# Optimization experiments

Hardware: AMD Instinct MI355X
Metric: run time of the kernel (lower is better)

The kernel has to match this reference:

```python
import jax, jax.numpy as jnp
import numpy as np

EPS = 1e-5
NEG_INF = -1e30


def layer_norm_seq(x, gamma, beta):
    # Faithful to the custom LayerNorm: normalizes over dim=1 (the T axis of
    # [B, T, C]) with UNBIASED variance (torch.var default), then scales by
    # gamma/beta of shape [C] broadcast over the last axis.
    m = jnp.mean(x, axis=1, keepdims=True)
    v = jnp.var(x, axis=1, keepdims=True, ddof=1)
    return gamma * (x - m) / jnp.sqrt(v + EPS) + beta


def setup_inputs() -> dict:
    key = jax.random.key(0)
    B, T, C, H = 4, 1024, 1024, 16
    hd = C // H  # 64
    ks = jax.random.split(key, 10)
    s_in = 1.0 / np.sqrt(C)
    s_ff = 1.0 / np.sqrt(4 * C)
    return {
        "x": jax.random.normal(ks[0], (B, T, C), dtype=jnp.float32),
        # NOTE: Head uses self.key(x) for BOTH q and k; the query Linear is
        # dead code, so only key/value weights are materialized.
        "Wk": jax.random.uniform(ks[1], (H, C, hd), minval=-s_in, maxval=s_in, dtype=jnp.float32),
        "Wv": jax.random.uniform(ks[2], (H, C, hd), minval=-s_in, maxval=s_in, dtype=jnp.float32),
        "Wp": jax.random.uniform(ks[3], (C, C), minval=-s_in, maxval=s_in, dtype=jnp.float32),
        "bp": jnp.zeros((C,), dtype=jnp.float32),
        "W1": jax.random.uniform(ks[4], (4 * C, C), minval=-s_in, maxval=s_in, dtype=jnp.float32),
        "b1": jnp.zeros((4 * C,), dtype=jnp.float32),
        "W2": jax.random.uniform(ks[5], (C, 4 * C), minval=-s_ff, maxval=s_ff, dtype=jnp.float32),
        "b2": jnp.zeros((C,), dtype=jnp.float32),
        "g1": jnp.ones((C,), dtype=jnp.float32),
        "beta1": jnp.zeros((C,), dtype=jnp.float32),
        "g2": jnp.ones((C,), dtype=jnp.float32),
        "beta2": jnp.zeros((C,), dtype=jnp.float32),
    }


def reference(x, Wk, Wv, Wp, bp, W1, b1, W2, b2, g1, beta1, g2, beta2):
    B, T, C = x.shape
    H, _, hd = Wk.shape
    scale = hd ** -0.5

    # --- self-attention sublayer (pre-LN over sequence axis) ---
    h = layer_norm_seq(x, g1, beta1)
    # q and k BOTH use the key projection (faithful to the original bug).
    qk = jnp.einsum("btc,hcd->bhtd", h, Wk)          # [B,H,T,hd]
    v = jnp.einsum("btc,hcd->bhtd", h, Wv)           # [B,H,T,hd]
    wei = jnp.einsum("bhtd,bhsd->bhts", qk, qk) * scale  # [B,H,T,T]
    causal = jnp.tril(jnp.ones((T, T), dtype=bool))
    wei = jnp.where(causal, wei, NEG_INF)
    wei = jax.nn.softmax(wei, axis=-1)
    attn = jnp.einsum("bhts,bhsd->bthd", wei, v).reshape(B, T, C)
    attn = attn @ Wp.T + bp
    x = x + attn

    # --- feed-forward sublayer ---
    h2 = layer_norm_seq(x, g2, beta2)
    ff = jax.nn.relu(h2 @ W1.T + b1) @ W2.T + b2
    return x + ff
```

## Files before the change

### kernel.cpp

```cpp
#include <hip/hip_runtime.h>
#include <stdint.h>


#define BDIM 256

typedef __attribute__((ext_vector_type(8))) __bf16 bf16x8;
typedef __attribute__((ext_vector_type(4))) float f32x4;

__device__ __forceinline__ unsigned short f2bf(float f) {
    unsigned u = __float_as_uint(f);
    u += 0x7fff + ((u >> 16) & 1);
    return (unsigned short)(u >> 16);
}

__device__ __forceinline__ void gload_lds16(const void* g, void* l) {
    __builtin_amdgcn_global_load_lds(
        (const __attribute__((address_space(1))) void*)g,
        (__attribute__((address_space(3))) void*)l, 16, 0, 0);
}

__global__ void k_cast_bf16(const float* __restrict__ in, unsigned short* __restrict__ out, int n4) {
    int i = blockIdx.x * BDIM + threadIdx.x;
    if (i >= n4) return;
    float4 v = ((const float4*)in)[i];
    ushort4 o;
    o.x = f2bf(v.x); o.y = f2bf(v.y); o.z = f2bf(v.z); o.w = f2bf(v.w);
    ((ushort4*)out)[i] = o;
}

__global__ void k_headT(const float* __restrict__ W, unsigned short* __restrict__ out) {
    __shared__ float tile[64][65];
    const int tid = threadIdx.x;
    const int c0 = blockIdx.x * 64, h = blockIdx.y;
    const float* src = W + ((long)h << 16) + (long)c0 * 64;
    #pragma unroll
    for (int j = 0; j < 16; ++j) {
        int idx = j * 256 + tid;
        tile[idx >> 6][idx & 63] = src[idx];
    }
    __syncthreads();
    #pragma unroll
    for (int j = 0; j < 16; ++j) {
        int idx = j * 256 + tid;
        int d = idx >> 6, c = idx & 63;
        out[(long)(h * 64 + d) * 1024 + c0 + c] = f2bf(tile[c][d]);
    }
}

__global__ void k_ln_part(const float* __restrict__ x, float* __restrict__ psum, float* __restrict__ psq) {
    int c = blockIdx.x * BDIM + threadIdx.x;
    int tc = blockIdx.y, b = blockIdx.z;
    const float* p = x + ((long)b << 20) + ((long)tc * 128) * 1024 + c;
    float s = 0.f, ss = 0.f;
    for (int t = 0; t < 128; ++t) {
        float v = p[t * 1024];
        s += v; ss += v * v;
    }
    int o = (b * 8 + tc) * 1024 + c;
    psum[o] = s; psq[o] = ss;
}

__global__ void k_ln_fin(const float* __restrict__ psum, const float* __restrict__ psq,
                         float* __restrict__ mean, float* __restrict__ rstd) {
    int i = blockIdx.x * BDIM + threadIdx.x;
    int b = i >> 10, c = i & 1023;
    float s = 0.f, ss = 0.f;
    for (int j = 0; j < 8; ++j) {
        s  += psum[(b * 8 + j) * 1024 + c];
        ss += psq[(b * 8 + j) * 1024 + c];
    }
    float m = s * (1.0f / 1024.0f);
    float var = (ss - 1024.0f * m * m) * (1.0f / 1023.0f);
    mean[i] = m;
    rstd[i] = rsqrtf(var + 1e-5f);
}

__global__ void k_ln_apply(const float* __restrict__ x, const float* __restrict__ mean,
                           const float* __restrict__ rstd, const float* __restrict__ g,
                           const float* __restrict__ beta, unsigned short* __restrict__ out) {
    int i = blockIdx.x * BDIM + threadIdx.x;
    int flat = i << 2;
    int b = flat >> 20, c = flat & 1023;
    float4 xv = ((const float4*)x)[i];
    float4 mv = *(const float4*)&mean[(b << 10) + c];
    float4 rv = *(const float4*)&rstd[(b << 10) + c];
    float4 gv = *(const float4*)&g[c];
    float4 bv = *(const float4*)&beta[c];
    ushort4 o;
    o.x = f2bf(gv.x * (xv.x - mv.x) * rv.x + bv.x);
    o.y = f2bf(gv.y * (xv.y - mv.y) * rv.y + bv.y);
    o.z = f2bf(gv.z * (xv.z - mv.z) * rv.z + bv.z);
    o.w = f2bf(gv.w * (xv.w - mv.w) * rv.w + bv.w);
    ((ushort4*)out)[i] = o;
}

__global__ void k_addbias(const float* __restrict__ res, const float* __restrict__ bias,
                          float* __restrict__ out) {
    int i = blockIdx.x * BDIM + threadIdx.x;
    int c = (i << 2) & 1023;
    float4 r = ((const float4*)res)[i];
    float4 bv = *(const float4*)&bias[c];
    r.x += bv.x; r.y += bv.y; r.z += bv.z; r.w += bv.w;
    ((float4*)out)[i] = r;
}

template <int EPI>
__global__ __launch_bounds__(256, 3) void k_gemm_bt(
    const unsigned short* __restrict__ A, const unsigned short* __restrict__ B,
    void* __restrict__ Cv, const float* __restrict__ bias, const float* __restrict__ res,
    int N, int K, int ldA, int ldB, long sA, long sB, long sC)
{
    __shared__ __align__(16) unsigned short As[2][128 * 32];
    __shared__ __align__(16) unsigned short Bs[2][128 * 32];
    const int tid = threadIdx.x;
    const int wave = tid >> 6, lane = tid & 63;
    const long bz = blockIdx.z;
    const int m0 = blockIdx.y * 128, n0 = blockIdx.x * 128;

    const int srow = wave * 16 + (lane >> 2);
    const int kbs = (lane & 3) ^ ((srow >> 1) & 3);
    const unsigned short* gA0 = A + bz * sA + (long)(m0 + srow) * ldA + kbs * 8;
    const unsigned short* gB0 = B + bz * sB + (long)(n0 + srow) * ldB + kbs * 8;
    const long rowoffA = (long)64 * ldA;
    const long rowoffB = (long)64 * ldB;
    const int lofs = wave * 512;

    f32x4 acc[4][4] = {};
    const int wm = (wave >> 1) * 64, wn = (wave & 1) * 64;
    const int lr = lane & 15, lg = lane >> 4;
    const int aoff = (lg ^ ((lr >> 1) & 3)) * 8;

    auto stage = [&](int kt, int buf) {
        gload_lds16(gA0 + kt, &As[buf][lofs]);
        gload_lds16(gA0 + rowoffA + kt, &As[buf][2048 + lofs]);
        gload_lds16(gB0 + kt, &Bs[buf][lofs]);
        gload_lds16(gB0 + rowoffB + kt, &Bs[buf][2048 + lofs]);
    };

    stage(0, 0);
    asm volatile("s_waitcnt vmcnt(0)" ::: "memory");
    __builtin_amdgcn_s_barrier();
    __builtin_amdgcn_sched_barrier(0);

    int cur = 0;
    for (int kt = 0; kt < K; kt += 32) {
        const int nxt = cur ^ 1;
        if (kt + 32 < K) stage(kt + 32, nxt);
        bf16x8 af[4], bfr[4];
        #pragma unroll
        for (int i = 0; i < 4; ++i) {
            af[i]  = *(const bf16x8*)&As[cur][(wm + i * 16 + lr) * 32 + aoff];
            bfr[i] = *(const bf16x8*)&Bs[cur][(wn + i * 16 + lr) * 32 + aoff];
        }
        #pragma unroll
        for (int i = 0; i < 4; ++i)
            #pragma unroll
            for (int j = 0; j < 4; ++j)
                acc[i][j] = __builtin_amdgcn_mfma_f32_16x16x32_bf16(af[i], bfr[j], acc[i][j], 0, 0, 0);
        asm volatile("s_waitcnt vmcnt(0)" ::: "memory");
        __builtin_amdgcn_s_barrier();
        __builtin_amdgcn_sched_barrier(0);
        cur = nxt;
    }

    const int cr0 = lg * 4;
    #pragma unroll
    for (int mi = 0; mi < 4; ++mi) {
        #pragma unroll
        for (int r = 0; r < 4; ++r) {
            const int row = m0 + wm + mi * 16 + cr0 + r;
            const long rb = bz * sC + (long)row * N;
            #pragma unroll
            for (int nj = 0; nj < 4; ++nj) {
                const int col = n0 + wn + nj * 16 + lr;
                float v = acc[mi][nj][r];
                if (EPI == 0) {
                    ((unsigned short*)Cv)[rb + col] = f2bf(v);
                } else if (EPI == 1) {
                    ((float*)Cv)[rb + col] = v + bias[col] + res[rb + col];
                } else {
                    v += bias[col];
                    ((unsigned short*)Cv)[rb + col] = f2bf(v > 0.f ? v : 0.f);
                }
            }
        }
    }
}

template <int EPI>
__global__ __launch_bounds__(512, 2) void k_gemm256(
    const unsigned short* __restrict__ A, const unsigned short* __restrict__ B,
    void* __restrict__ Cv, const float* __restrict__ bias,
    int N, int K, int ldA, int ldB)
{
    __shared__ __align__(16) unsigned short As[2][2][128 * 64];
    __shared__ __align__(16) unsigned short Bs[2][2][128 * 64];
    const int tid = threadIdx.x;
    const int wv = tid >> 6, l = tid & 63;
    const int m0 = blockIdx.y * 256, n0 = blockIdx.x * 256;
    const long koff = (long)blockIdx.z * K;

    const int lr = l & 15, lg = l >> 4;

    const int srow = wv * 16 + (l >> 3);
    const int g0 = (l & 7) ^ (l >> 4);
    const int g1 = (l & 7) ^ (4 + (l >> 4));
    const unsigned short* pA = A + koff + (long)(m0 + srow) * ldA;
    const unsigned short* pB = B + koff + (long)(n0 + srow) * ldB;
    const long l8A = (long)8 * ldA, l128A = (long)128 * ldA;
    const long l8B = (long)8 * ldB, l128B = (long)128 * ldB;
    const int dst0 = wv * 1024;

    auto stage = [&](int k0, int d) {
        #pragma unroll
        for (int h = 0; h < 2; ++h) {
            gload_lds16(pA + (long)h * l128A + k0 + g0 * 8, &As[d][h][dst0]);
            gload_lds16(pA + (long)h * l128A + l8A + k0 + g1 * 8, &As[d][h][dst0 + 512]);
            gload_lds16(pB + (long)h * l128B + k0 + g0 * 8, &Bs[d][h][dst0]);
            gload_lds16(pB + (long)h * l128B + l8B + k0 + g1 * 8, &Bs[d][h][dst0 + 512]);
        }
    };

    f32x4 acc[8][4] = {};
    const int wh = wv >> 2;
    const int bh = (wv & 3) >> 1;
    const int brow0 = (wv & 1) * 64;
    const int swz = (lr >> 1) & 7;

    stage(0, 0);

    const int nt = K >> 6;
    int cur = 0;
    for (int t = 0; t < nt; ++t) {
        asm volatile("s_waitcnt vmcnt(0)" ::: "memory");
        __builtin_amdgcn_s_barrier();
        __builtin_amdgcn_sched_barrier(0);
        if (t + 1 < nt) stage((t + 1) << 6, cur ^ 1);
        const unsigned short* Ah = &As[cur][wh][0];
        const unsigned short* Bh = &Bs[cur][bh][0];
        #pragma unroll
        for (int ks = 0; ks < 2; ++ks) {
            const int kb = ((ks * 4 + lg) ^ swz) * 8;
            bf16x8 af[8], bfr[4];
            #pragma unroll
            for (int fm = 0; fm < 8; ++fm)
                af[fm] = *(const bf16x8*)&Ah[(fm * 16 + lr) * 64 + kb];
            #pragma unroll
            for (int fn = 0; fn < 4; ++fn)
                bfr[fn] = *(const bf16x8*)&Bh[(brow0 + fn * 16 + lr) * 64 + kb];
            asm volatile("s_waitcnt lgkmcnt(0)" ::: "memory");
            __builtin_amdgcn_sched_barrier(0);
            __builtin_amdgcn_s_setprio(1);
            #pragma unroll
            for (int fm = 0; fm < 8; ++fm)
                #pragma unroll
                for (int fn = 0; fn < 4; ++fn)
                    acc[fm][fn] = __builtin_amdgcn_mfma_f32_16x16x32_bf16(af[fm], bfr[fn], acc[fm][fn], 0, 0, 0);
            __builtin_amdgcn_s_setprio(0);
            __builtin_amdgcn_sched_barrier(0);
        }
        cur ^= 1;
    }

    const int wm = (wv >> 2) * 128, wn = (wv & 3) * 64;
    #pragma unroll
    for (int fm = 0; fm < 8; ++fm) {
        #pragma unroll
        for (int r = 0; r < 4; ++r) {
            const int row = m0 + wm + fm * 16 + lg * 4 + r;
            const long rb = (long)row * N;
            #pragma unroll
            for (int fn = 0; fn < 4; ++fn) {
                const int col = n0 + wn + fn * 16 + lr;
                float v = acc[fm][fn][r];
                if (EPI == 2) {
                    v += bias[col];
                    ((unsigned short*)Cv)[rb + col] = f2bf(v > 0.f ? v : 0.f);
                } else {
                    atomicAdd(&((float*)Cv)[rb + col], v);
                }
            }
        }
    }
}

#define CEXP 0.18033688f
#define PSTRIDE 72

__global__ __launch_bounds__(256, 2) void k_attn(
    const unsigned short* __restrict__ qk, const unsigned short* __restrict__ vt,
    unsigned short* __restrict__ ctx)
{
    __shared__ __align__(16) unsigned short Ks[64 * 64];
    __shared__ __align__(16) unsigned short Vs[64 * 64];
    __shared__ __align__(16) unsigned short P[4][16 * PSTRIDE];
    const int tid = threadIdx.x;
    const int wave = tid >> 6, lane = tid & 63;
    const int bh = blockIdx.x >> 3, pairIdx = blockIdx.x & 7;
    const int b = bh >> 4, h = bh & 15;
    const int lr = lane & 15, lg = lane >> 4;

    const int swz = (lr & 7) << 4;
    const int cby0 = (lg * 16) ^ swz;
    const int cby1 = (64 + lg * 16) ^ swz;
    const int srow_l = lane >> 3;
    const int scol = ((lane & 7) * 8) ^ (srow_l << 3);

    unsigned short* Pw = P[wave];
    char* KsB = (char*)Ks;
    char* VsB = (char*)Vs;
    const unsigned short* qbase = qk + ((long)b << 20) + h * 64;
    const unsigned short* vb    = vt + ((long)(b * 16 + h) << 16);

    #pragma unroll 1
    for (int phase = 0; phase < 2; ++phase) {
        const int qb = phase ? (15 - pairIdx) : pairIdx;
        const int q0 = qb << 6;
        const int qw = q0 + wave * 16;

        const unsigned short* qrow = qbase + (long)(qw + lr) * 1024 + lg * 8;
        const bf16x8 aq0 = *(const bf16x8*)qrow;
        const bf16x8 aq1 = *(const bf16x8*)(qrow + 32);

        f32x4 acc[4] = {};
        float mrow[4] = {-1e30f, -1e30f, -1e30f, -1e30f};
        float lrow[4] = {0.f, 0.f, 0.f, 0.f};

        for (int c = 0; c <= qb; ++c) {
            const int k0 = c << 6;
            __syncthreads();
            #pragma unroll
            for (int i = 0; i < 2; ++i) {
                const int row = i * 32 + wave * 8 + srow_l;
                gload_lds16(qbase + (long)(k0 + row) * 1024 + scol,
                            KsB + i * 4096 + wave * 1024);
                gload_lds16(vb + (long)row * 1024 + k0 + scol,
                            VsB + i * 4096 + wave * 1024);
            }
            __syncthreads();

            f32x4 s[4];
            #pragma unroll
            for (int t = 0; t < 4; ++t) {
                const int r = t * 16 + lr;
                bf16x8 bk0 = *(const bf16x8*)(KsB + r * 128 + cby0);
                bf16x8 bk1 = *(const bf16x8*)(KsB + r * 128 + cby1);
                f32x4 z = {};
                z = __builtin_amdgcn_mfma_f32_16x16x32_bf16(aq0, bk0, z, 0, 0, 0);
                s[t] = __builtin_amdgcn_mfma_f32_16x16x32_bf16(aq1, bk1, z, 0, 0, 0);
            }
            if (c == qb) {
                #pragma unroll
                for (int t = 0; t < 4; ++t) {
                    const int col = t * 16 + lr;
                    #pragma unroll
                    for (int r = 0; r < 4; ++r)
                        if (col > wave * 16 + lg * 4 + r) s[t][r] = -1e30f;
                }
            }
            float fac[4];
            #pragma unroll
            for (int r = 0; r < 4; ++r) {
                float v = fmaxf(fmaxf(s[0][r], s[1][r]), fmaxf(s[2][r], s[3][r]));
                v = fmaxf(v, __shfl_xor(v, 1));
                v = fmaxf(v, __shfl_xor(v, 2));
                v = fmaxf(v, __shfl_xor(v, 4));
                v = fmaxf(v, __shfl_xor(v, 8));
                float mn = fmaxf(mrow[r], v);
                fac[r] = exp2f((mrow[r] - mn) * CEXP);
                mrow[r] = mn;
            }
            float psum[4] = {0.f, 0.f, 0.f, 0.f};
            #pragma unroll
            for (int t = 0; t < 4; ++t) {
                #pragma unroll
                for (int r = 0; r < 4; ++r) {
                    float p = exp2f((s[t][r] - mrow[r]) * CEXP);
                    psum[r] += p;
                    Pw[(lg * 4 + r) * PSTRIDE + t * 16 + lr] = f2bf(p);
                }
            }
            #pragma unroll
            for (int r = 0; r < 4; ++r) {
                float v = psum[r];
                v += __shfl_xor(v, 1); v += __shfl_xor(v, 2);
                v += __shfl_xor(v, 4); v += __shfl_xor(v, 8);
                lrow[r] = lrow[r] * fac[r] + v;
            }
            #pragma unroll
            for (int ni = 0; ni < 4; ++ni)
                #pragma unroll
                for (int r = 0; r < 4; ++r)
                    acc[ni][r] *= fac[r];
            const bf16x8 pa0 = *(const bf16x8*)&Pw[lr * PSTRIDE + lg * 8];
            const bf16x8 pa1 = *(const bf16x8*)&Pw[lr * PSTRIDE + 32 + lg * 8];
            #pragma unroll
            for (int ni = 0; ni < 4; ++ni) {
                const int vr = ni * 16 + lr;
                bf16x8 bv0 = *(const bf16x8*)(VsB + vr * 128 + cby0);
                bf16x8 bv1 = *(const bf16x8*)(VsB + vr * 128 + cby1);
                acc[ni] = __builtin_amdgcn_mfma_f32_16x16x32_bf16(pa0, bv0, acc[ni], 0, 0, 0);
                acc[ni] = __builtin_amdgcn_mfma_f32_16x16x32_bf16(pa1, bv1, acc[ni], 0, 0, 0);
            }
        }

        unsigned short* crow = ctx + ((long)(b * 1024 + qw)) * 1024 + h * 64;
        #pragma unroll
        for (int r = 0; r < 4; ++r) {
            const float inv = 1.0f / lrow[r];
            #pragma unroll
            for (int ni = 0; ni < 4; ++ni)
                crow[(long)(lg * 4 + r) * 1024 + ni * 16 + lr] = f2bf(acc[ni][r] * inv);
        }
    }
}

extern "C" void kernel_launch(void* const* d_in, const int* in_sizes, int n_in,
                              void* d_out, int out_size, void* d_ws, size_t ws_size,
                              hipStream_t stream)
{
    const float* x   = (const float*)d_in[0];
    const float* Wk  = (const float*)d_in[1];
    const float* Wv  = (const float*)d_in[2];
    const float* Wp  = (const float*)d_in[3];
    const float* bp  = (const float*)d_in[4];
    const float* W1  = (const float*)d_in[5];
    const float* b1  = (const float*)d_in[6];
    const float* W2  = (const float*)d_in[7];
    const float* b2  = (const float*)d_in[8];
    const float* g1  = (const float*)d_in[9];
    const float* be1 = (const float*)d_in[10];
    const float* g2  = (const float*)d_in[11];
    const float* be2 = (const float*)d_in[12];
    float* out = (float*)d_out;

    char* ws = (char*)d_ws;
    const long MB = 1024 * 1024;
    unsigned short* BkT = (unsigned short*)(ws);
    unsigned short* WvT = (unsigned short*)(ws + 2 * MB);
    unsigned short* WpB = (unsigned short*)(ws + 4 * MB);
    unsigned short* W1B = (unsigned short*)(ws + 6 * MB);
    unsigned short* W2B = (unsigned short*)(ws + 14 * MB);
    unsigned short* hB  = (unsigned short*)(ws + 22 * MB);
    unsigned short* qkB = (unsigned short*)(ws + 30 * MB);
    unsigned short* VtB = (unsigned short*)(ws + 38 * MB);
    unsigned short* ctx = (unsigned short*)(ws + 46 * MB);
    unsigned short* ff1 = (unsigned short*)(ws + 30 * MB);
    float* x2   = (float*)(ws + 62 * MB);
    float* psum = (float*)(ws + 78 * MB);
    float* psq  = (float*)(ws + 78 * MB + 128 * 1024);
    float* mean = (float*)(ws + 78 * MB + 256 * 1024);
    float* rstd = (float*)(ws + 78 * MB + 272 * 1024);

    k_cast_bf16<<<1024, BDIM, 0, stream>>>(Wp, WpB, 262144);
    k_cast_bf16<<<4096, BDIM, 0, stream>>>(W1, W1B, 1048576);
    k_cast_bf16<<<4096, BDIM, 0, stream>>>(W2, W2B, 1048576);
    k_headT<<<dim3(16, 16), BDIM, 0, stream>>>(Wk, BkT);
    k_headT<<<dim3(16, 16), BDIM, 0, stream>>>(Wv, WvT);

    k_ln_part<<<dim3(4, 8, 4), BDIM, 0, stream>>>(x, psum, psq);
    k_ln_fin<<<16, BDIM, 0, stream>>>(psum, psq, mean, rstd);
    k_ln_apply<<<4096, BDIM, 0, stream>>>(x, mean, rstd, g1, be1, hB);

    k_gemm_bt<0><<<dim3(8, 32, 1), BDIM, 0, stream>>>(hB, BkT, qkB, nullptr, nullptr, 1024, 1024, 1024, 1024, 0, 0, 0);
    k_gemm_bt<0><<<dim3(8, 8, 4), BDIM, 0, stream>>>(WvT, hB, VtB, nullptr, nullptr, 1024, 1024, 1024, 1024, 0, MB, MB);

    k_attn<<<512, BDIM, 0, stream>>>(qkB, VtB, ctx);

    k_gemm_bt<1><<<dim3(8, 32, 1), BDIM, 0, stream>>>(ctx, WpB, x2, bp, x, 1024, 1024, 1024, 1024, 0, 0, 0);

    k_ln_part<<<dim3(4, 8, 4), BDIM, 0, stream>>>(x2, psum, psq);
    k_ln_fin<<<16, BDIM, 0, stream>>>(psum, psq, mean, rstd);
    k_ln_apply<<<4096, BDIM, 0, stream>>>(x2, mean, rstd, g2, be2, hB);

    k_gemm256<2><<<dim3(16, 16, 1), 512, 0, stream>>>(hB, W1B, ff1, b1, 4096, 1024, 1024, 1024);

    k_addbias<<<4096, BDIM, 0, stream>>>(x2, b2, out);
    k_gemm256<3><<<dim3(4, 16, 4), 512, 0, stream>>>(ff1, W2B, out, nullptr, 1024, 1024, 4096, 4096);
}
```

Before: 403.0 us.

## Deepen GEMM prefetch, split MFMA into quadrants, and remap workgroups across XCDs

The 256x256 GEMM now prefetches two k-tiles ahead and waits on a partial vmcnt instead of draining all loads, so global-to-LDS copies overlap more compute. Fragment loads and MFMA work are split into four quadrant phases separated by barriers, in a ping-pong style meant to interleave LDS reads with matrix ops. Workgroup IDs are remapped with a stride of 8 so neighbouring tiles land on the same XCD for L2 reuse. The extra barriers add sync overhead, and the remap assumes the grid size divides by 8.

Result: no change. 399.3 us (-0.9%).

```diff
diff --git a/kernel.cpp b/kernel.cpp
--- a/kernel.cpp
+++ b/kernel.cpp
@@ -197,7 +197,12 @@
     __shared__ __align__(16) unsigned short Bs[2][2][128 * 64];
     const int tid = threadIdx.x;
     const int wv = tid >> 6, l = tid & 63;
-    const int m0 = blockIdx.y * 256, n0 = blockIdx.x * 256;
+
+    const int gx = gridDim.x;
+    const int nwg = gx * gridDim.y;
+    int lin = blockIdx.y * gx + blockIdx.x;
+    lin = (lin & 7) * (nwg >> 3) + (lin >> 3);
+    const int m0 = (lin / gx) * 256, n0 = (lin % gx) * 256;
     const long koff = (long)blockIdx.z * K;
 
     const int lr = l & 15, lg = l >> 4;
@@ -223,43 +228,95 @@
 
     f32x4 acc[8][4] = {};
     const int wh = wv >> 2;
-    const int bh = (wv & 3) >> 1;
+    const int bhf = (wv & 3) >> 1;
     const int brow0 = (wv & 1) * 64;
     const int swz = (lr >> 1) & 7;
 
+    const int nt = K >> 6;
     stage(0, 0);
-
-    const int nt = K >> 6;
-    int cur = 0;
+    stage(64, 1);
+
     for (int t = 0; t < nt; ++t) {
-        asm volatile("s_waitcnt vmcnt(0)" ::: "memory");
+        const int d = t & 1;
+        if (t + 1 < nt) { asm volatile("s_waitcnt vmcnt(8)" ::: "memory"); }
+        else            { asm volatile("s_waitcnt vmcnt(0)" ::: "memory"); }
         __builtin_amdgcn_s_barrier();
         __builtin_amdgcn_sched_barrier(0);
-        if (t + 1 < nt) stage((t + 1) << 6, cur ^ 1);
-        const unsigned short* Ah = &As[cur][wh][0];
-        const unsigned short* Bh = &Bs[cur][bh][0];
-        #pragma unroll
-        for (int ks = 0; ks < 2; ++ks) {
-            const int kb = ((ks * 4 + lg) ^ swz) * 8;
-            bf16x8 af[8], bfr[4];
-            #pragma unroll
-            for (int fm = 0; fm < 8; ++fm)
-                af[fm] = *(const bf16x8*)&Ah[(fm * 16 + lr) * 64 + kb];
-            #pragma unroll
-            for (int fn = 0; fn < 4; ++fn)
-                bfr[fn] = *(const bf16x8*)&Bh[(brow0 + fn * 16 + lr) * 64 + kb];
-            asm volatile("s_waitcnt lgkmcnt(0)" ::: "memory");
-            __builtin_amdgcn_sched_barrier(0);
-            __builtin_amdgcn_s_setprio(1);
-            #pragma unroll
-            for (int fm = 0; fm < 8; ++fm)
-                #pragma unroll
-                for (int fn = 0; fn < 4; ++fn)
-                    acc[fm][fn] = __builtin_amdgcn_mfma_f32_16x16x32_bf16(af[fm], bfr[fn], acc[fm][fn], 0, 0, 0);
-            __builtin_amdgcn_s_setprio(0);
-            __builtin_amdgcn_sched_barrier(0);
-        }
-        cur ^= 1;
+        const unsigned short* Ah = &As[d][wh][0];
+        const unsigned short* Bh = &Bs[d][bhf][0];
+
+        bf16x8 aLo[4][2], aHi[4][2], b01[2][2], b23[2][2];
+        #pragma unroll
+        for (int fm = 0; fm < 4; ++fm)
+            #pragma unroll
+            for (int ks = 0; ks < 2; ++ks)
+                aLo[fm][ks] = *(const bf16x8*)&Ah[(fm * 16 + lr) * 64 + (((ks * 4 + lg) ^ swz) * 8)];
+        #pragma unroll
+        for (int fn = 0; fn < 2; ++fn)
+            #pragma unroll
+            for (int ks = 0; ks < 2; ++ks)
+                b01[fn][ks] = *(const bf16x8*)&Bh[(brow0 + fn * 16 + lr) * 64 + (((ks * 4 + lg) ^ swz) * 8)];
+        asm volatile("s_waitcnt lgkmcnt(0)" ::: "memory");
+        __builtin_amdgcn_sched_barrier(0);
+        __builtin_amdgcn_s_setprio(1);
+        #pragma unroll
+        for (int fm = 0; fm < 4; ++fm)
+            #pragma unroll
+            for (int fn = 0; fn < 2; ++fn)
+                #pragma unroll
+                for (int ks = 0; ks < 2; ++ks)
+                    acc[fm][fn] = __builtin_amdgcn_mfma_f32_16x16x32_bf16(aLo[fm][ks], b01[fn][ks], acc[fm][fn], 0, 0, 0);
+        __builtin_amdgcn_s_setprio(0);
+        __builtin_amdgcn_sched_barrier(0);
+        __builtin_amdgcn_s_barrier();
+        #pragma unroll
+        for (int fn = 0; fn < 2; ++fn)
+            #pragma unroll
+            for (int ks = 0; ks < 2; ++ks)
+                b23[fn][ks] = *(const bf16x8*)&Bh[(brow0 + (fn + 2) * 16 + lr) * 64 + (((ks * 4 + lg) ^ swz) * 8)];
+        asm volatile("s_waitcnt lgkmcnt(0)" ::: "memory");
+        __builtin_amdgcn_sched_barrier(0);
+        __builtin_amdgcn_s_setprio(1);
+        #pragma unroll
+        for (int fm = 0; fm < 4; ++fm)
+            #pragma unroll
+            for (int fn = 0; fn < 2; ++fn)
+                #pragma unroll
+                for (int ks = 0; ks < 2; ++ks)
+                    acc[fm][fn + 2] = __builtin_amdgcn_mfma_f32_16x16x32_bf16(aLo[fm][ks], b23[fn][ks], acc[fm][fn + 2], 0, 0, 0);
+        __builtin_amdgcn_s_setprio(0);
+        __builtin_amdgcn_sched_barrier(0);
+        __builtin_amdgcn_s_barrier();
+        #pragma unroll
+        for (int fm = 0; fm < 4; ++fm)
+            #pragma unroll
+            for (int ks = 0; ks < 2; ++ks)
+                aHi[fm][ks] = *(const bf16x8*)&Ah[((fm + 4) * 16 + lr) * 64 + (((ks * 4 + lg) ^ swz) * 8)];
+        asm volatile("s_waitcnt lgkmcnt(0)" ::: "memory");
+        __builtin_amdgcn_sched_barrier(0);
+        __builtin_amdgcn_s_setprio(1);
+        #pragma unroll
+        for (int fm = 0; fm < 4; ++fm)
+            #pragma unroll
+            for (int fn = 0; fn < 2; ++fn)
+                #pragma unroll
+                for (int ks = 0; ks < 2; ++ks)
+                    acc[fm + 4][fn + 2] = __builtin_amdgcn_mfma_f32_16x16x32_bf16(aHi[fm][ks], b23[fn][ks], acc[fm + 4][fn + 2], 0, 0, 0);
+        __builtin_amdgcn_s_setprio(0);
+        __builtin_amdgcn_sched_barrier(0);
+        __builtin_amdgcn_s_barrier();
+        __builtin_amdgcn_s_setprio(1);
+        #pragma unroll
+        for (int fm = 0; fm < 4; ++fm)
+            #pragma unroll
+            for (int fn = 0; fn < 2; ++fn)
+                #pragma unroll
+                for (int ks = 0; ks < 2; ++ks)
+                    acc[fm + 4][fn] = __builtin_amdgcn_mfma_f32_16x16x32_bf16(aHi[fm][ks], b01[fn][ks], acc[fm + 4][fn], 0, 0, 0);
+        __builtin_amdgcn_s_setprio(0);
+        __builtin_amdgcn_sched_barrier(0);
+        __builtin_amdgcn_s_barrier();
+        if (t + 2 < nt) stage((t + 2) << 6, d);
     }
 
     const int wm = (wv >> 2) * 128, wn = (wv & 3) * 64;
```
